# Optimization experiments

Measured on AMD Instinct MI355X. Metric: run time of the kernel, lower is better.

The kernel has to match this reference:

```python
import jax, jax.numpy as jnp
import numpy as np

IMG_SIZE = 100
N_QUBITS = 4
N_BLOCKS = 5
STRIDE = 2
OUT = (IMG_SIZE - STRIDE) // STRIDE + 1  # 50
PAIRS = ((0, 1), (1, 2), (2, 3), (3, 0))  # circular CU3 connectivity


def _u3(p):
    # p = (theta, phi, lam) -> 2x2 complex64 U3 matrix
    th, ph, la = p[0], p[1], p[2]
    c = jnp.cos(th / 2).astype(jnp.complex64)
    s = jnp.sin(th / 2).astype(jnp.complex64)
    ei = lambda a: jnp.exp(1j * a.astype(jnp.complex64))
    return jnp.stack([jnp.stack([c, -ei(la) * s]),
                      jnp.stack([ei(ph) * s, ei(ph + la) * c])])


def _cu3(p):
    u = _u3(p)
    U4 = jnp.zeros((4, 4), jnp.complex64)
    U4 = U4.at[0, 0].set(1.0).at[1, 1].set(1.0).at[2:, 2:].set(u)
    return U4


def _apply_1q(state, U, w):
    # state: [P,2,2,2,2]; wire w -> axis 1+w
    st = jnp.moveaxis(state, 1 + w, -1)
    st = jnp.einsum('...b,ab->...a', st, U)
    return jnp.moveaxis(st, -1, 1 + w)


def _apply_2q(state, U4, ctrl, tgt):
    st = jnp.moveaxis(state, (1 + ctrl, 1 + tgt), (-2, -1))
    sh = st.shape
    st = st.reshape(sh[:-2] + (4,))
    st = jnp.einsum('...b,ab->...a', st, U4)
    return jnp.moveaxis(st.reshape(sh), (-2, -1), (1 + ctrl, 1 + tgt))


def _forward(x, u3_params, cu3_params, W, b):
    img = x.reshape(IMG_SIZE, IMG_SIZE)
    # extract 2x2 patches; patch p = c*OUT + r, pixels row-major within patch
    patches = img.reshape(OUT, STRIDE, OUT, STRIDE).transpose(0, 2, 1, 3).reshape(-1, N_QUBITS)
    # RY(x_i)|0> = [cos(x/2), sin(x/2)] -> product state, built directly
    half = patches / 2
    v = jnp.stack([jnp.cos(half), jnp.sin(half)], -1).astype(jnp.complex64)  # [P,4,2]
    state = jnp.einsum('pa,pb,pc,pd->pabcd', v[:, 0], v[:, 1], v[:, 2], v[:, 3])
    for blk in range(N_BLOCKS):
        for w in range(N_QUBITS):
            state = _apply_1q(state, _u3(u3_params[blk, w]), w)
        for k, (c_, t_) in enumerate(PAIRS):
            state = _apply_2q(state, _cu3(cu3_params[blk, k]), c_, t_)
    probs = (state.real ** 2 + state.imag ** 2).reshape(-1, 16)  # [P,16]
    bits = (np.arange(16)[None, :] >> (N_QUBITS - 1 - np.arange(N_QUBITS)[:, None])) & 1
    signs = jnp.asarray(1.0 - 2.0 * bits, jnp.float32)  # [4,16] PauliZ signs (wire 0 = MSB)
    ez = probs @ signs.T  # [P,4] <Z_w>
    # source: stack over (c, r) then squeeze + transpose(0,2) -> [4, r, c]
    feat = ez.reshape(OUT, OUT, N_QUBITS).transpose(2, 1, 0).reshape(N_QUBITS, OUT * OUT)
    logits = feat @ W.T + b  # [4, 2] (channels act as batch, per source)
    return jax.nn.log_softmax(logits, -1)


def setup_inputs() -> dict:
    key = jax.random.key(0)
    k1, k2, k3, k4, k5 = jax.random.split(key, 5)
    return {
        'x': jax.random.uniform(k1, (1, IMG_SIZE, IMG_SIZE), jnp.float32),
        'u3_params': jax.random.normal(k2, (N_BLOCKS, N_QUBITS, 3), jnp.float32),
        'cu3_params': jax.random.normal(k3, (N_BLOCKS, N_QUBITS, 3), jnp.float32),
        'W': jax.random.normal(k4, (2, OUT * OUT), jnp.float32) * 0.02,
        'b': jax.random.normal(k5, (2,), jnp.float32) * 0.02,
    }


def reference(x, u3_params, cu3_params, W, b):
    return _forward(x, u3_params, cu3_params, W, b)
```

## Files before the change

### kernel.cpp

```cpp
#include <hip/hip_runtime.h>

#define IMG 100
#define OUTD 50
#define NPATCH 2500
#define NB 5
#define NGATE (NB * 8)

__device__ __forceinline__ float2 cmul(float2 a, float2 b) {
    return make_float2(a.x * b.x - a.y * b.y, a.x * b.y + a.y * b.x);
}
__device__ __forceinline__ float2 cadd(float2 a, float2 b) {
    return make_float2(a.x + b.x, a.y + b.y);
}

__global__ __launch_bounds__(64) void qconv_kernel(
    const float* __restrict__ img,
    const float* __restrict__ u3p,
    const float* __restrict__ cu3p,
    float* __restrict__ ez_ws)
{
    __shared__ float2 gm[NGATE][4];
    const int tid = threadIdx.x;

    if (tid < NGATE) {
        const int blk = tid >> 3;
        const int idx = tid & 7;
        const float* pp = (idx < 4) ? &u3p[(blk * 4 + idx) * 3]
                                    : &cu3p[(blk * 4 + (idx - 4)) * 3];
        const float th = pp[0], ph = pp[1], la = pp[2];
        float s, c, sl, cl, sp, cp, spl, cpl;
        sincosf(th * 0.5f, &s, &c);
        sincosf(la, &sl, &cl);
        sincosf(ph, &sp, &cp);
        sincosf(ph + la, &spl, &cpl);
        gm[tid][0] = make_float2(c, 0.0f);
        gm[tid][1] = make_float2(-cl * s, -sl * s);
        gm[tid][2] = make_float2(cp * s, sp * s);
        gm[tid][3] = make_float2(cpl * c, spl * c);
    }
    __syncthreads();

    const int p = blockIdx.x * blockDim.x + tid;
    if (p >= NPATCH) return;

    const int rb = p / OUTD;
    const int cb = p - rb * OUTD;
    const int i0 = 2 * rb, j0 = 2 * cb;

    float x[4];
    x[0] = img[i0 * IMG + j0];
    x[1] = img[i0 * IMG + j0 + 1];
    x[2] = img[(i0 + 1) * IMG + j0];
    x[3] = img[(i0 + 1) * IMG + j0 + 1];

    float v[4][2];
#pragma unroll
    for (int w = 0; w < 4; ++w) {
        sincosf(x[w] * 0.5f, &v[w][1], &v[w][0]);
    }

    float2 amp[16];
#pragma unroll
    for (int i = 0; i < 16; ++i) {
        const int b0 = (i >> 3) & 1, b1 = (i >> 2) & 1, b2 = (i >> 1) & 1, b3 = i & 1;
        amp[i] = make_float2(v[0][b0] * v[1][b1] * v[2][b2] * v[3][b3], 0.0f);
    }

    const int pc[4] = {0, 1, 2, 3};
    const int pt[4] = {1, 2, 3, 0};

#pragma unroll
    for (int blk = 0; blk < NB; ++blk) {
#pragma unroll
        for (int w = 0; w < 4; ++w) {
            const float2 m0 = gm[blk * 8 + w][0];
            const float2 m1 = gm[blk * 8 + w][1];
            const float2 m2 = gm[blk * 8 + w][2];
            const float2 m3 = gm[blk * 8 + w][3];
            const int sw = 1 << (3 - w);
#pragma unroll
            for (int i = 0; i < 16; ++i) {
                if ((i & sw) == 0) {
                    const float2 a0 = amp[i], a1 = amp[i + sw];
                    amp[i]      = cadd(cmul(m0, a0), cmul(m1, a1));
                    amp[i + sw] = cadd(cmul(m2, a0), cmul(m3, a1));
                }
            }
        }
#pragma unroll
        for (int k = 0; k < 4; ++k) {
            const float2 m0 = gm[blk * 8 + 4 + k][0];
            const float2 m1 = gm[blk * 8 + 4 + k][1];
            const float2 m2 = gm[blk * 8 + 4 + k][2];
            const float2 m3 = gm[blk * 8 + 4 + k][3];
            const int sc = 1 << (3 - pc[k]);
            const int st = 1 << (3 - pt[k]);
#pragma unroll
            for (int i = 0; i < 16; ++i) {
                if ((i & sc) != 0 && (i & st) == 0) {
                    const float2 a0 = amp[i], a1 = amp[i + st];
                    amp[i]      = cadd(cmul(m0, a0), cmul(m1, a1));
                    amp[i + st] = cadd(cmul(m2, a0), cmul(m3, a1));
                }
            }
        }
    }

    float ez[4] = {0.f, 0.f, 0.f, 0.f};
#pragma unroll
    for (int i = 0; i < 16; ++i) {
        const float pr = amp[i].x * amp[i].x + amp[i].y * amp[i].y;
#pragma unroll
        for (int w = 0; w < 4; ++w)
            ez[w] += ((i >> (3 - w)) & 1) ? -pr : pr;
    }
#pragma unroll
    for (int w = 0; w < 4; ++w) ez_ws[p * 4 + w] = ez[w];
}

__global__ __launch_bounds__(256) void head_kernel(
    const float* __restrict__ ez_ws,
    const float* __restrict__ W,
    const float* __restrict__ b,
    float* __restrict__ out)
{
    const int tid = threadIdx.x;
    float acc[8] = {0.f, 0.f, 0.f, 0.f, 0.f, 0.f, 0.f, 0.f};

    for (int j = tid; j < NPATCH; j += 256) {
        const int cbj = j / OUTD;
        const int rbj = j - cbj * OUTD;
        const int p = rbj * OUTD + cbj;
        const float w0 = W[j];
        const float w1 = W[NPATCH + j];
#pragma unroll
        for (int q = 0; q < 4; ++q) {
            const float f = ez_ws[p * 4 + q];
            acc[q * 2 + 0] += f * w0;
            acc[q * 2 + 1] += f * w1;
        }
    }

    __shared__ float sdata[8 * 256];
#pragma unroll
    for (int i = 0; i < 8; ++i) sdata[i * 256 + tid] = acc[i];
    __syncthreads();
    for (int s = 128; s > 0; s >>= 1) {
        if (tid < s) {
#pragma unroll
            for (int i = 0; i < 8; ++i)
                sdata[i * 256 + tid] += sdata[i * 256 + tid + s];
        }
        __syncthreads();
    }
    if (tid == 0) {
        const float b0 = b[0], b1 = b[1];
#pragma unroll
        for (int q = 0; q < 4; ++q) {
            const float l0 = sdata[(q * 2 + 0) * 256] + b0;
            const float l1 = sdata[(q * 2 + 1) * 256] + b1;
            const float m = fmaxf(l0, l1);
            const float lse = m + logf(expf(l0 - m) + expf(l1 - m));
            out[q * 2 + 0] = l0 - lse;
            out[q * 2 + 1] = l1 - lse;
        }
    }
}

extern "C" void kernel_launch(void* const* d_in, const int* in_sizes, int n_in,
                              void* d_out, int out_size, void* d_ws, size_t ws_size,
                              hipStream_t stream) {
    const float* img  = (const float*)d_in[0];
    const float* u3p  = (const float*)d_in[1];
    const float* cu3p = (const float*)d_in[2];
    const float* W    = (const float*)d_in[3];
    const float* b    = (const float*)d_in[4];
    float* out   = (float*)d_out;
    float* ez_ws = (float*)d_ws;

    qconv_kernel<<<(NPATCH + 63) / 64, 64, 0, stream>>>(img, u3p, cu3p, ez_ws);
    head_kernel<<<1, 256, 0, stream>>>(ez_ws, W, b, out);
}
```

Measured before the change: 77.22 us.

## Fuse linear head into qconv kernel via wave shuffles and atomic last-block finish

Merges the separate head kernel into the circuit-simulation kernel. Each wave multiplies its expectation values by the matching weights, reduces them with shuffles and atomically adds into a small logits buffer. A ticket counter lets the last block apply the bias and log-softmax. It also switches sincos/exp/log to fast intrinsics, and adds a memset launch to zero the workspace, at some cost in accuracy and atomic ordering nondeterminism.

```diff
diff --git a/kernel.cpp b/kernel.cpp
--- a/kernel.cpp
+++ b/kernel.cpp
@@ -5,6 +5,7 @@
 #define NPATCH 2500
 #define NB 5
 #define NGATE (NB * 8)
+#define NBLK ((NPATCH + 63) / 64)
 
 __device__ __forceinline__ float2 cmul(float2 a, float2 b) {
     return make_float2(a.x * b.x - a.y * b.y, a.x * b.y + a.y * b.x);
@@ -13,11 +14,15 @@
     return make_float2(a.x + b.x, a.y + b.y);
 }
 
-__global__ __launch_bounds__(64) void qconv_kernel(
+__global__ __launch_bounds__(64) void qconv_fused(
     const float* __restrict__ img,
     const float* __restrict__ u3p,
     const float* __restrict__ cu3p,
-    float* __restrict__ ez_ws)
+    const float* __restrict__ W,
+    const float* __restrict__ bias,
+    float* __restrict__ ws_logits,
+    unsigned* __restrict__ ws_count,
+    float* __restrict__ out)
 {
     __shared__ float2 gm[NGATE][4];
     const int tid = threadIdx.x;
@@ -29,10 +34,10 @@
                                     : &cu3p[(blk * 4 + (idx - 4)) * 3];
         const float th = pp[0], ph = pp[1], la = pp[2];
         float s, c, sl, cl, sp, cp, spl, cpl;
-        sincosf(th * 0.5f, &s, &c);
-        sincosf(la, &sl, &cl);
-        sincosf(ph, &sp, &cp);
-        sincosf(ph + la, &spl, &cpl);
+        __sincosf(th * 0.5f, &s, &c);
+        __sincosf(la, &sl, &cl);
+        __sincosf(ph, &sp, &cp);
+        __sincosf(ph + la, &spl, &cpl);
         gm[tid][0] = make_float2(c, 0.0f);
         gm[tid][1] = make_float2(-cl * s, -sl * s);
         gm[tid][2] = make_float2(cp * s, sp * s);
@@ -40,24 +45,24 @@
     }
     __syncthreads();
 
-    const int p = blockIdx.x * blockDim.x + tid;
-    if (p >= NPATCH) return;
+    const int p = blockIdx.x * 64 + tid;
+    const bool active = (p < NPATCH);
+    const int pcl = active ? p : (NPATCH - 1);
 
-    const int rb = p / OUTD;
-    const int cb = p - rb * OUTD;
+    const int rb = pcl / OUTD;
+    const int cb = pcl - rb * OUTD;
     const int i0 = 2 * rb, j0 = 2 * cb;
 
-    float x[4];
-    x[0] = img[i0 * IMG + j0];
-    x[1] = img[i0 * IMG + j0 + 1];
-    x[2] = img[(i0 + 1) * IMG + j0];
-    x[3] = img[(i0 + 1) * IMG + j0 + 1];
+    float x0 = img[i0 * IMG + j0];
+    float x1 = img[i0 * IMG + j0 + 1];
+    float x2 = img[(i0 + 1) * IMG + j0];
+    float x3 = img[(i0 + 1) * IMG + j0 + 1];
 
     float v[4][2];
-#pragma unroll
-    for (int w = 0; w < 4; ++w) {
-        sincosf(x[w] * 0.5f, &v[w][1], &v[w][0]);
-    }
+    __sincosf(x0 * 0.5f, &v[0][1], &v[0][0]);
+    __sincosf(x1 * 0.5f, &v[1][1], &v[1][0]);
+    __sincosf(x2 * 0.5f, &v[2][1], &v[2][0]);
+    __sincosf(x3 * 0.5f, &v[3][1], &v[3][0]);
 
     float2 amp[16];
 #pragma unroll
@@ -66,7 +71,6 @@
         amp[i] = make_float2(v[0][b0] * v[1][b1] * v[2][b2] * v[3][b3], 0.0f);
     }
 
-    const int pc[4] = {0, 1, 2, 3};
     const int pt[4] = {1, 2, 3, 0};
 
 #pragma unroll
@@ -93,7 +97,7 @@
             const float2 m1 = gm[blk * 8 + 4 + k][1];
             const float2 m2 = gm[blk * 8 + 4 + k][2];
             const float2 m3 = gm[blk * 8 + 4 + k][3];
-            const int sc = 1 << (3 - pc[k]);
+            const int sc = 1 << (3 - k);
             const int st = 1 << (3 - pt[k]);
 #pragma unroll
             for (int i = 0; i < 16; ++i) {
@@ -114,55 +118,44 @@
         for (int w = 0; w < 4; ++w)
             ez[w] += ((i >> (3 - w)) & 1) ? -pr : pr;
     }
+
+    const int j = cb * OUTD + rb;
+    const float w0 = active ? W[j] : 0.0f;
+    const float w1 = active ? W[NPATCH + j] : 0.0f;
+    float part[8];
 #pragma unroll
-    for (int w = 0; w < 4; ++w) ez_ws[p * 4 + w] = ez[w];
-}
-
-__global__ __launch_bounds__(256) void head_kernel(
-    const float* __restrict__ ez_ws,
-    const float* __restrict__ W,
-    const float* __restrict__ b,
-    float* __restrict__ out)
-{
-    const int tid = threadIdx.x;
-    float acc[8] = {0.f, 0.f, 0.f, 0.f, 0.f, 0.f, 0.f, 0.f};
-
-    for (int j = tid; j < NPATCH; j += 256) {
-        const int cbj = j / OUTD;
-        const int rbj = j - cbj * OUTD;
-        const int p = rbj * OUTD + cbj;
-        const float w0 = W[j];
-        const float w1 = W[NPATCH + j];
-#pragma unroll
-        for (int q = 0; q < 4; ++q) {
-            const float f = ez_ws[p * 4 + q];
-            acc[q * 2 + 0] += f * w0;
-            acc[q * 2 + 1] += f * w1;
-        }
+    for (int q = 0; q < 4; ++q) {
+        part[q * 2 + 0] = ez[q] * w0;
+        part[q * 2 + 1] = ez[q] * w1;
     }
 
-    __shared__ float sdata[8 * 256];
 #pragma unroll
-    for (int i = 0; i < 8; ++i) sdata[i * 256 + tid] = acc[i];
-    __syncthreads();
-    for (int s = 128; s > 0; s >>= 1) {
-        if (tid < s) {
+    for (int off = 32; off > 0; off >>= 1) {
 #pragma unroll
-            for (int i = 0; i < 8; ++i)
-                sdata[i * 256 + tid] += sdata[i * 256 + tid + s];
-        }
-        __syncthreads();
+        for (int i = 0; i < 8; ++i)
+            part[i] += __shfl_down(part[i], off, 64);
     }
+
     if (tid == 0) {
-        const float b0 = b[0], b1 = b[1];
 #pragma unroll
-        for (int q = 0; q < 4; ++q) {
-            const float l0 = sdata[(q * 2 + 0) * 256] + b0;
-            const float l1 = sdata[(q * 2 + 1) * 256] + b1;
-            const float m = fmaxf(l0, l1);
-            const float lse = m + logf(expf(l0 - m) + expf(l1 - m));
-            out[q * 2 + 0] = l0 - lse;
-            out[q * 2 + 1] = l1 - lse;
+        for (int i = 0; i < 8; ++i) atomicAdd(&ws_logits[i], part[i]);
+        __threadfence();
+        const unsigned ticket = atomicAdd(ws_count, 1u);
+        if (ticket == (unsigned)(gridDim.x - 1)) {
+            __threadfence();
+            float l[8];
+#pragma unroll
+            for (int i = 0; i < 8; ++i) l[i] = atomicAdd(&ws_logits[i], 0.0f);
+            const float b0 = bias[0], b1 = bias[1];
+#pragma unroll
+            for (int q = 0; q < 4; ++q) {
+                const float l0 = l[q * 2 + 0] + b0;
+                const float l1 = l[q * 2 + 1] + b1;
+                const float m = fmaxf(l0, l1);
+                const float lse = m + __logf(__expf(l0 - m) + __expf(l1 - m));
+                out[q * 2 + 0] = l0 - lse;
+                out[q * 2 + 1] = l1 - lse;
+            }
         }
     }
 }
@@ -175,9 +168,12 @@
     const float* cu3p = (const float*)d_in[2];
     const float* W    = (const float*)d_in[3];
     const float* b    = (const float*)d_in[4];
-    float* out   = (float*)d_out;
-    float* ez_ws = (float*)d_ws;
+    float* out = (float*)d_out;
 
-    qconv_kernel<<<(NPATCH + 63) / 64, 64, 0, stream>>>(img, u3p, cu3p, ez_ws);
-    head_kernel<<<1, 256, 0, stream>>>(ez_ws, W, b, out);
+    float* ws_logits = (float*)d_ws;
+    unsigned* ws_count = (unsigned*)((char*)d_ws + 32);
+
+    hipMemsetAsync(d_ws, 0, 64, stream);
+    qconv_fused<<<NBLK, 64, 0, stream>>>(img, u3p, cu3p, W, b,
+                                         ws_logits, ws_count, out);
 }
```

New measurement: 78.98 us. 1.02x slower.
